# Performance work log

Measured on AMD Instinct MI355X. Metric: run time of the kernel, lower is better.

Reference implementation:

```python
import jax, jax.numpy as jnp
import numpy as np

RADIUS = 0.2
NSAMPLE = 32
USE_XYZ = True


def setup_inputs() -> dict:
    key = jax.random.key(0)
    k1, k2, k3 = jax.random.split(key, 3)
    B, N, NP, C = 16, 4096, 1024, 64
    xyz = jax.random.uniform(k1, (B, N, 3), dtype=jnp.float32)
    new_xyz = jax.random.uniform(k2, (B, NP, 3), dtype=jnp.float32)
    points = jax.random.normal(k3, (B, C, N), dtype=jnp.float32)
    return {"xyz": xyz, "new_xyz": new_xyz, "points": points}


def ball_query(radius, nsample, xyz, new_xyz):
    """Replicates the CUDA ball_query: for each center, the first `nsample`
    points (in index order) with squared distance < radius^2. Unfilled slots
    are set to the first in-radius index (0 if none in radius)."""
    B, N, _ = xyz.shape
    NP = new_xyz.shape[1]
    # [B, NP, N] squared distances
    d2 = jnp.sum((new_xyz[:, :, None, :] - xyz[:, None, :, :]) ** 2, axis=-1)
    mask = d2 < (radius * radius)
    order = jnp.cumsum(mask.astype(jnp.int32), axis=-1)  # 1-based rank among in-radius pts
    cnt = order[..., -1]                                  # [B, NP] in-radius count
    # slot for each point: rank-1 if it is one of the first nsample in-radius, else dummy
    slot = jnp.where(mask & (order <= nsample), order - 1, nsample)
    bb = jnp.arange(B, dtype=jnp.int32)[:, None, None]
    pp = jnp.arange(NP, dtype=jnp.int32)[None, :, None]
    nn = jnp.broadcast_to(jnp.arange(N, dtype=jnp.int32)[None, None, :], (B, NP, N))
    idx = jnp.zeros((B, NP, nsample + 1), dtype=jnp.int32).at[bb, pp, slot].set(nn)
    idx = idx[..., :nsample]
    # replicate first in-radius index into unfilled slots (stays 0 if cnt == 0)
    filled = jnp.arange(nsample)[None, None, :] < jnp.minimum(cnt, nsample)[..., None]
    idx = jnp.where(filled, idx, idx[..., :1])
    return idx


def reference(xyz, new_xyz, points):
    idx = ball_query(RADIUS, NSAMPLE, xyz, new_xyz)          # [B, NP, NS] int32
    # gather xyz: [B, NP, NS, 3] -> [B, 3, NP, NS]
    grouped_xyz = jax.vmap(lambda x, i: x[i])(xyz, idx)
    grouped_xyz = jnp.transpose(grouped_xyz, (0, 3, 1, 2))
    # centroid subtract
    grouped_xyz = grouped_xyz - jnp.transpose(new_xyz, (0, 2, 1))[..., None]
    # gather features: points [B, C, N] -> [B, C, NP, NS]
    grouped_points = jax.vmap(lambda p, i: p[:, i])(points, idx)
    if USE_XYZ:
        new_points = jnp.concatenate([grouped_xyz, grouped_points], axis=1)
    else:
        new_points = grouped_points
    return new_points
```

## Files before the change

kernel.cpp:

```cpp
#include <hip/hip_runtime.h>
#include <hip/hip_bf16.h>

constexpr int B  = 16;
constexpr int N  = 4096;
constexpr int NP = 1024;
constexpr int C  = 64;
constexpr int NS = 32;
constexpr int OC = C + 3;
constexpr float R2 = 0.2f * 0.2f;

typedef float v4f __attribute__((ext_vector_type(4)));
typedef int   v4i __attribute__((ext_vector_type(4)));

__global__ __launch_bounds__(256)
void ball_query_kernel(const float* __restrict__ xyz,
                       const float* __restrict__ new_xyz,
                       float* __restrict__ out,
                       int* __restrict__ ws_idx)
{
    const int wid  = (blockIdx.x << 2) + (threadIdx.x >> 6);
    const int lane = threadIdx.x & 63;
    const int b = wid >> 10;
    const int p = wid & (NP - 1);

    const float qx = new_xyz[wid * 3 + 0];
    const float qy = new_xyz[wid * 3 + 1];
    const float qz = new_xyz[wid * 3 + 2];

    const float* xb = xyz + (size_t)b * N * 3;

    float* out_x = out + (((size_t)b * OC + 0) * NP + p) * NS;
    float* out_y = out + (((size_t)b * OC + 1) * NP + p) * NS;
    float* out_z = out + (((size_t)b * OC + 2) * NP + p) * NS;
    int*   idx_p = ws_idx + (size_t)wid * NS;

    float fdx = xb[0] - qx;
    float fdy = xb[1] - qy;
    float fdz = xb[2] - qz;
    int   fidx = 0;

    int cnt = 0;
    for (int base = 0; base < N && cnt < NS; base += 128) {
        const int j0 = base + lane;
        const int j1 = base + 64 + lane;

        const float x0 = xb[j0 * 3 + 0];
        const float y0 = xb[j0 * 3 + 1];
        const float z0 = xb[j0 * 3 + 2];
        const float x1 = xb[j1 * 3 + 0];
        const float y1 = xb[j1 * 3 + 1];
        const float z1 = xb[j1 * 3 + 2];

        const float dx0 = x0 - qx, dy0 = y0 - qy, dz0 = z0 - qz;
        const float dx1 = x1 - qx, dy1 = y1 - qy, dz1 = z1 - qz;
        const float d20 = __fadd_rn(__fadd_rn(__fmul_rn(dx0, dx0),
                                              __fmul_rn(dy0, dy0)),
                                    __fmul_rn(dz0, dz0));
        const float d21 = __fadd_rn(__fadd_rn(__fmul_rn(dx1, dx1),
                                              __fmul_rn(dy1, dy1)),
                                    __fmul_rn(dz1, dz1));
        const bool in0 = d20 < R2;
        const bool in1 = d21 < R2;
        const unsigned long long m0 = __ballot(in0);
        const unsigned long long m1 = __ballot(in1);

        if (cnt == 0) {
            if (m0 != 0ull) {
                const int fl = __ffsll(m0) - 1;
                fdx = __shfl(dx0, fl, 64);
                fdy = __shfl(dy0, fl, 64);
                fdz = __shfl(dz0, fl, 64);
                fidx = base + fl;
            } else if (m1 != 0ull) {
                const int fl = __ffsll(m1) - 1;
                fdx = __shfl(dx1, fl, 64);
                fdy = __shfl(dy1, fl, 64);
                fdz = __shfl(dz1, fl, 64);
                fidx = base + 64 + fl;
            }
        }

        const unsigned long long below = (1ull << lane) - 1ull;
        if (in0) {
            const int slot = cnt + (int)__popcll(m0 & below);
            if (slot < NS) {
                idx_p[slot] = j0;
                out_x[slot] = dx0;
                out_y[slot] = dy0;
                out_z[slot] = dz0;
            }
        }
        const int c0 = cnt + (int)__popcll(m0);
        if (in1) {
            const int slot = c0 + (int)__popcll(m1 & below);
            if (slot < NS) {
                idx_p[slot] = j1;
                out_x[slot] = dx1;
                out_y[slot] = dy1;
                out_z[slot] = dz1;
            }
        }
        cnt = c0 + (int)__popcll(m1);
    }

    const int cntc = cnt < NS ? cnt : NS;
    if (lane >= cntc && lane < NS) {
        idx_p[lane] = fidx;
        out_x[lane] = fdx;
        out_y[lane] = fdy;
        out_z[lane] = fdz;
    }
}

__global__ __launch_bounds__(256)
void group_points_kernel(const float* __restrict__ points,
                         const int* __restrict__ ws_idx,
                         float* __restrict__ out)
{
    __shared__ float s_row[2 * N];

    const int bc = blockIdx.x;
    const int b  = bc >> 5;
    const int c2 = (bc & 31) * 2;

    const v4f* row4 = (const v4f*)(points + ((size_t)b * C + c2) * N);
    v4f* s4 = (v4f*)s_row;
    #pragma unroll
    for (int i = threadIdx.x; i < 2 * N / 4; i += 256)
        s4[i] = row4[i];
    __syncthreads();

    const v4i* idx4 = (const v4i*)(ws_idx + (size_t)b * NP * NS);
    v4f* out0 = (v4f*)(out + ((size_t)b * OC + 3 + c2) * NP * NS);
    v4f* out1 = (v4f*)(out + ((size_t)b * OC + 4 + c2) * NP * NS);

    for (int t = threadIdx.x; t < NP * NS / 4; t += 256) {
        const v4i id = idx4[t];
        v4f va, vb;
        va.x = s_row[id.x];
        va.y = s_row[id.y];
        va.z = s_row[id.z];
        va.w = s_row[id.w];
        vb.x = s_row[N + id.x];
        vb.y = s_row[N + id.y];
        vb.z = s_row[N + id.z];
        vb.w = s_row[N + id.w];
        __builtin_nontemporal_store(va, &out0[t]);
        __builtin_nontemporal_store(vb, &out1[t]);
    }
}

extern "C" void kernel_launch(void* const* d_in, const int* in_sizes, int n_in,
                              void* d_out, int out_size, void* d_ws, size_t ws_size,
                              hipStream_t stream)
{
    const float* xyz     = (const float*)d_in[0];
    const float* new_xyz = (const float*)d_in[1];
    const float* points  = (const float*)d_in[2];
    float* out = (float*)d_out;
    int* ws_idx = (int*)d_ws;

    ball_query_kernel<<<(B * NP) / 4, 256, 0, stream>>>(xyz, new_xyz, out, ws_idx);

    group_points_kernel<<<B * (C / 2), 256, 0, stream>>>(points, ws_idx, out);
}
```

Measured before the change: 196.8 us.

## Vectorize ball query scan with 4 points per lane, prefetch, and LDS hit staging

The ball query kernel now processes 256 points per iteration, with each lane loading 4 points as three float4 vector loads. The next tile is prefetched while the current one is evaluated. Hits are written to a per-wave shared-memory buffer as (index, dx, dy, dz) records, ranked with mbcnt. One coalesced pass then writes the idx and xyz outputs, and the first-hit fill is read back from LDS instead of being tracked with shuffles. The goal is to replace scalar strided loads and scattered global writes with vector loads and contiguous stores. The cost is more registers and scanning in coarser 256-point steps, which can overshoot the early exit.

```diff
diff --git a/kernel.cpp b/kernel.cpp
--- a/kernel.cpp
+++ b/kernel.cpp
@@ -1,5 +1,4 @@
 #include <hip/hip_runtime.h>
-#include <hip/hip_bf16.h>
 
 constexpr int B  = 16;
 constexpr int N  = 4096;
@@ -12,13 +11,22 @@
 typedef float v4f __attribute__((ext_vector_type(4)));
 typedef int   v4i __attribute__((ext_vector_type(4)));
 
+__device__ __forceinline__ int mbcnt64(unsigned long long m) {
+    return (int)__builtin_amdgcn_mbcnt_hi(
+        (unsigned)(m >> 32),
+        __builtin_amdgcn_mbcnt_lo((unsigned)m, 0u));
+}
+
 __global__ __launch_bounds__(256)
 void ball_query_kernel(const float* __restrict__ xyz,
                        const float* __restrict__ new_xyz,
                        float* __restrict__ out,
                        int* __restrict__ ws_idx)
 {
-    const int wid  = (blockIdx.x << 2) + (threadIdx.x >> 6);
+    __shared__ __align__(16) float s_hits[4][NS][4];
+
+    const int wv   = threadIdx.x >> 6;
+    const int wid  = (blockIdx.x << 2) + wv;
     const int lane = threadIdx.x & 63;
     const int b = wid >> 10;
     const int p = wid & (NP - 1);
@@ -28,87 +36,76 @@
     const float qz = new_xyz[wid * 3 + 2];
 
     const float* xb = xyz + (size_t)b * N * 3;
+    const v4f* src = (const v4f*)xb;
+    const int l3 = lane * 3;
+
+    float (*hits)[4] = s_hits[wv];
+
+    v4f A  = src[l3 + 0];
+    v4f Bv = src[l3 + 1];
+    v4f Cv = src[l3 + 2];
+
+    int cnt = 0;
+    int tile = 0;
+    for (;;) {
+        v4f nA, nB, nC;
+        const bool more = (tile + 1) < (N / 256);
+        if (more) {
+            const v4f* s2 = src + (tile + 1) * 192 + l3;
+            nA = s2[0]; nB = s2[1]; nC = s2[2];
+        }
+
+        const float dx0 = A.x  - qx, dy0 = A.y  - qy, dz0 = A.z  - qz;
+        const float dx1 = A.w  - qx, dy1 = Bv.x - qy, dz1 = Bv.y - qz;
+        const float dx2 = Bv.z - qx, dy2 = Bv.w - qy, dz2 = Cv.x - qz;
+        const float dx3 = Cv.y - qx, dy3 = Cv.z - qy, dz3 = Cv.w - qz;
+        const float d20 = __fadd_rn(__fadd_rn(__fmul_rn(dx0,dx0),__fmul_rn(dy0,dy0)),__fmul_rn(dz0,dz0));
+        const float d21 = __fadd_rn(__fadd_rn(__fmul_rn(dx1,dx1),__fmul_rn(dy1,dy1)),__fmul_rn(dz1,dz1));
+        const float d22 = __fadd_rn(__fadd_rn(__fmul_rn(dx2,dx2),__fmul_rn(dy2,dy2)),__fmul_rn(dz2,dz2));
+        const float d23 = __fadd_rn(__fadd_rn(__fmul_rn(dx3,dx3),__fmul_rn(dy3,dy3)),__fmul_rn(dz3,dz3));
+        const bool in0 = d20 < R2;
+        const bool in1 = d21 < R2;
+        const bool in2 = d22 < R2;
+        const bool in3 = d23 < R2;
+        const unsigned long long m0 = __ballot(in0);
+        const unsigned long long m1 = __ballot(in1);
+        const unsigned long long m2 = __ballot(in2);
+        const unsigned long long m3 = __ballot(in3);
+
+        const int T = mbcnt64(m0) + mbcnt64(m1) + mbcnt64(m2) + mbcnt64(m3);
+        const int jb = tile * 256 + lane * 4;
+
+        int sl = cnt + T;
+        if (in0) { if (sl < NS) { v4f h; h.x = __int_as_float(jb + 0); h.y = dx0; h.z = dy0; h.w = dz0; *(v4f*)hits[sl] = h; } ++sl; }
+        if (in1) { if (sl < NS) { v4f h; h.x = __int_as_float(jb + 1); h.y = dx1; h.z = dy1; h.w = dz1; *(v4f*)hits[sl] = h; } ++sl; }
+        if (in2) { if (sl < NS) { v4f h; h.x = __int_as_float(jb + 2); h.y = dx2; h.z = dy2; h.w = dz2; *(v4f*)hits[sl] = h; } ++sl; }
+        if (in3) { if (sl < NS) { v4f h; h.x = __int_as_float(jb + 3); h.y = dx3; h.z = dy3; h.w = dz3; *(v4f*)hits[sl] = h; } ++sl; }
+
+        cnt += (int)(__popcll(m0) + __popcll(m1) + __popcll(m2) + __popcll(m3));
+        if (cnt >= NS || !more) break;
+        A = nA; Bv = nB; Cv = nC; ++tile;
+    }
 
     float* out_x = out + (((size_t)b * OC + 0) * NP + p) * NS;
     float* out_y = out + (((size_t)b * OC + 1) * NP + p) * NS;
     float* out_z = out + (((size_t)b * OC + 2) * NP + p) * NS;
     int*   idx_p = ws_idx + (size_t)wid * NS;
 
-    float fdx = xb[0] - qx;
-    float fdy = xb[1] - qy;
-    float fdz = xb[2] - qz;
-    int   fidx = 0;
-
-    int cnt = 0;
-    for (int base = 0; base < N && cnt < NS; base += 128) {
-        const int j0 = base + lane;
-        const int j1 = base + 64 + lane;
-
-        const float x0 = xb[j0 * 3 + 0];
-        const float y0 = xb[j0 * 3 + 1];
-        const float z0 = xb[j0 * 3 + 2];
-        const float x1 = xb[j1 * 3 + 0];
-        const float y1 = xb[j1 * 3 + 1];
-        const float z1 = xb[j1 * 3 + 2];
-
-        const float dx0 = x0 - qx, dy0 = y0 - qy, dz0 = z0 - qz;
-        const float dx1 = x1 - qx, dy1 = y1 - qy, dz1 = z1 - qz;
-        const float d20 = __fadd_rn(__fadd_rn(__fmul_rn(dx0, dx0),
-                                              __fmul_rn(dy0, dy0)),
-                                    __fmul_rn(dz0, dz0));
-        const float d21 = __fadd_rn(__fadd_rn(__fmul_rn(dx1, dx1),
-                                              __fmul_rn(dy1, dy1)),
-                                    __fmul_rn(dz1, dz1));
-        const bool in0 = d20 < R2;
-        const bool in1 = d21 < R2;
-        const unsigned long long m0 = __ballot(in0);
-        const unsigned long long m1 = __ballot(in1);
-
-        if (cnt == 0) {
-            if (m0 != 0ull) {
-                const int fl = __ffsll(m0) - 1;
-                fdx = __shfl(dx0, fl, 64);
-                fdy = __shfl(dy0, fl, 64);
-                fdz = __shfl(dz0, fl, 64);
-                fidx = base + fl;
-            } else if (m1 != 0ull) {
-                const int fl = __ffsll(m1) - 1;
-                fdx = __shfl(dx1, fl, 64);
-                fdy = __shfl(dy1, fl, 64);
-                fdz = __shfl(dz1, fl, 64);
-                fidx = base + 64 + fl;
-            }
+    const int cntc = cnt < NS ? cnt : NS;
+    if (lane < NS) {
+        v4f h;
+        if (cnt > 0) {
+            h = *(const v4f*)hits[lane < cntc ? lane : 0];
+        } else {
+            h.x = __int_as_float(0);
+            h.y = xb[0] - qx;
+            h.z = xb[1] - qy;
+            h.w = xb[2] - qz;
         }
-
-        const unsigned long long below = (1ull << lane) - 1ull;
-        if (in0) {
-            const int slot = cnt + (int)__popcll(m0 & below);
-            if (slot < NS) {
-                idx_p[slot] = j0;
-                out_x[slot] = dx0;
-                out_y[slot] = dy0;
-                out_z[slot] = dz0;
-            }
-        }
-        const int c0 = cnt + (int)__popcll(m0);
-        if (in1) {
-            const int slot = c0 + (int)__popcll(m1 & below);
-            if (slot < NS) {
-                idx_p[slot] = j1;
-                out_x[slot] = dx1;
-                out_y[slot] = dy1;
-                out_z[slot] = dz1;
-            }
-        }
-        cnt = c0 + (int)__popcll(m1);
-    }
-
-    const int cntc = cnt < NS ? cnt : NS;
-    if (lane >= cntc && lane < NS) {
-        idx_p[lane] = fidx;
-        out_x[lane] = fdx;
-        out_y[lane] = fdy;
-        out_z[lane] = fdz;
+        idx_p[lane] = __float_as_int(h.x);
+        out_x[lane] = h.y;
+        out_y[lane] = h.z;
+        out_z[lane] = h.w;
     }
 }
 
```

Result: faster. 182.8 us (-7.1%).
